# Optimization experiments

Hardware: AMD Instinct MI355X
Metric: run time of the kernel (lower is better)

## Reference

```python
import jax, jax.numpy as jnp
import numpy as np

NUM_GRAPHS = 512
LEAKY_SLOPE = 0.01


def _gconv(x, src, dst, w, W_root, W_rel, b_rel):
    # PyG GraphConv: out = lin_rel(sum_j w_ij * x_j) + lin_root(x)
    msg = x[src] * w[:, None]                       # [E, d] gather + scale
    agg = jax.ops.segment_sum(msg, dst, num_segments=x.shape[0])  # scatter-add
    return agg @ W_rel + b_rel + x @ W_root


def setup_inputs() -> dict:
    key = jax.random.key(0)
    ks = jax.random.split(key, 12)
    N, E, D, H, C = 100000, 1250000, 64, 64, 8
    x_embeddings = jax.random.normal(ks[0], (N, D), dtype=jnp.float32)
    edge_index = jax.random.randint(ks[1], (2, E), 0, N, dtype=jnp.int64)
    weights = jax.random.uniform(ks[2], (E,), dtype=jnp.float32)
    batch = jnp.sort(jax.random.randint(ks[3], (N,), 0, NUM_GRAPHS, dtype=jnp.int64))
    s1 = 1.0 / np.sqrt(D)
    s2 = 1.0 / np.sqrt(H)
    W1_root = jax.random.uniform(ks[4], (D, H), jnp.float32, -s1, s1)
    W1_rel = jax.random.uniform(ks[5], (D, H), jnp.float32, -s1, s1)
    b1 = jax.random.uniform(ks[6], (H,), jnp.float32, -s1, s1)
    W2_root = jax.random.uniform(ks[7], (H, H), jnp.float32, -s2, s2)
    W2_rel = jax.random.uniform(ks[8], (H, H), jnp.float32, -s2, s2)
    b2 = jax.random.uniform(ks[9], (H,), jnp.float32, -s2, s2)
    Wl_root = jax.random.uniform(ks[10], (H, C), jnp.float32, -s2, s2)
    bl = jax.random.uniform(ks[11], (C,), jnp.float32, -s2, s2)
    return {"x_embeddings": x_embeddings, "edge_index": edge_index,
            "weights": weights, "batch": batch,
            "W1_root": W1_root, "W1_rel": W1_rel, "b1": b1,
            "W2_root": W2_root, "W2_rel": W2_rel, "b2": b2,
            "Wl_root": Wl_root, "bl": bl}


def reference(x_embeddings, edge_index, weights, batch,
              W1_root, W1_rel, b1, W2_root, W2_rel, b2, Wl_root, bl):
    src, dst = edge_index[0], edge_index[1]
    x = _gconv(x_embeddings, src, dst, weights, W1_root, W1_rel, b1)
    x = jax.nn.leaky_relu(x, LEAKY_SLOPE)
    x = _gconv(x, src, dst, weights, W2_root, W2_rel, b2)
    x = jax.nn.leaky_relu(x, LEAKY_SLOPE)
    # global_mean_pool over graph ids
    summed = jax.ops.segment_sum(x, batch, num_segments=NUM_GRAPHS)
    counts = jax.ops.segment_sum(jnp.ones((x.shape[0],), x.dtype), batch,
                                 num_segments=NUM_GRAPHS)
    pooled = summed / jnp.maximum(counts, 1.0)[:, None]
    # final GraphConv applied with no edges: agg = 0 -> W_root x + b_rel
    out = pooled @ Wl_root + bl
    return out
```

## Files before the change

kernel.cpp:

```cpp
#include <hip/hip_runtime.h>

#define LEAKY_SLOPE 0.01f
#define NUM_GRAPHS 512
#define TILE 4096
#define NB_MAX 512
#define POOL_SPAN 8

typedef __attribute__((ext_vector_type(8))) short short8;
typedef __attribute__((ext_vector_type(4))) float f32x4;

static __device__ __forceinline__ unsigned short f2bf(float f) {
    unsigned u = __float_as_uint(f);
    u += 0x7FFFu + ((u >> 16) & 1u);
    return (unsigned short)(u >> 16);
}
static __device__ __forceinline__ float bf2f(unsigned short h) {
    return __uint_as_float(((unsigned)h) << 16);
}

static __device__ __forceinline__ int wave_incl_scan(int v, int lane) {
#pragma unroll
    for (int off = 1; off < 64; off <<= 1) {
        int t = __shfl_up(v, off, 64);
        if (lane >= off) v += t;
    }
    return v;
}

__global__ __launch_bounds__(256)
void mega_prep(const int* __restrict__ dst, int* __restrict__ bucketCnt, int E,
               int NB, int histBlocks,
               const float* __restrict__ x, unsigned short* __restrict__ xB,
               int xElems , int xBlocks,
               const float* __restrict__ W1rel, const float* __restrict__ W1root,
               const float* __restrict__ W2rel, const float* __restrict__ W2root,
               unsigned short* __restrict__ Bt1, unsigned short* __restrict__ Bt2) {
    const int bid = blockIdx.x;
    if (bid < histBlocks) {
        __shared__ int h[NB_MAX];
        for (int t = threadIdx.x; t < NB_MAX; t += 256) h[t] = 0;
        __syncthreads();
        const int base = bid * TILE;
#pragma unroll
        for (int i = 0; i < TILE / 256; ++i) {
            int e = base + i * 256 + threadIdx.x;
            if (e < E) atomicAdd(&h[dst[e] >> 8], 1);
        }
        __syncthreads();
        for (int t = threadIdx.x; t < NB; t += 256)
            if (h[t]) atomicAdd(&bucketCnt[t], h[t]);
    } else if (bid < histBlocks + xBlocks) {
        int i = (bid - histBlocks) * 256 + threadIdx.x;
        if (i < xElems) {
            float4 f = ((const float4*)x)[i];
            ushort4 o = make_ushort4(f2bf(f.x), f2bf(f.y), f2bf(f.z), f2bf(f.w));
            ((ushort4*)xB)[i] = o;
        }
    } else {
        int b2 = bid - histBlocks - xBlocks;
        for (int idx = b2 * 2048 + threadIdx.x; idx < (b2 + 1) * 2048; idx += 256) {
            int which = idx >> 13;
            int j = idx & 8191;
            int n = j >> 7, k = j & 127;
            const float* Wr = which ? W2rel : W1rel;
            const float* Wo = which ? W2root : W1root;
            float v = (k < 64) ? Wr[k * 64 + n] : Wo[(k - 64) * 64 + n];
            (which ? Bt2 : Bt1)[j] = f2bf(v);
        }
    }
}

__global__ __launch_bounds__(512)
void bscan_kernel(const int* __restrict__ bucketCnt, int* __restrict__ bucketBase,
                  int* __restrict__ cursor, int* __restrict__ rowStart,
                  float* __restrict__ pooled, int N, int E, int NB) {
    __shared__ int ws[8];
    const int t = threadIdx.x, lane = t & 63, wid = t >> 6;
    int v = (t < NB) ? bucketCnt[t] : 0;
    int s = wave_incl_scan(v, lane);
    if (lane == 63) ws[wid] = s;
    __syncthreads();
    int add = 0;
    for (int i = 0; i < wid; ++i) add += ws[i];
    if (t < NB) {
        int excl = s + add - v;
        bucketBase[t] = excl;
        cursor[t] = excl;
    }
    if (t == 0) rowStart[N] = E;
    float4 z = make_float4(0.f, 0.f, 0.f, 0.f);
#pragma unroll
    for (int i = 0; i < 16; ++i)
        ((float4*)pooled)[t * 16 + i] = z;
}

__global__ __launch_bounds__(256)
void p1b_partition(const int* __restrict__ src, const int* __restrict__ dst,
                   const float* __restrict__ w, int* __restrict__ cursor,
                   int2* __restrict__ tmp, int E, int NB) {
    __shared__ int h[NB_MAX];
    __shared__ int cur[NB_MAX];
    __shared__ int lstart[NB_MAX];
    __shared__ int gbase[NB_MAX];
    __shared__ int ws[4];
    __shared__ int2 pay[TILE];
    __shared__ unsigned short bk[TILE];

    for (int t = threadIdx.x; t < NB_MAX; t += 256) h[t] = 0;
    __syncthreads();

    const int base = blockIdx.x * TILE;
    int   myb[TILE / 256];
    int   myp[TILE / 256];
    float myw[TILE / 256];
#pragma unroll
    for (int i = 0; i < TILE / 256; ++i) {
        int e = base + i * 256 + threadIdx.x;
        if (e < E) {
            int d = dst[e];
            myb[i] = d >> 8;
            myp[i] = src[e] | ((d & 255) << 20);
            myw[i] = w[e];
            atomicAdd(&h[myb[i]], 1);
        } else {
            myb[i] = -1;
        }
    }
    __syncthreads();

    {
        const int t = threadIdx.x, lane = t & 63, wid = t >> 6;
        int a = h[2 * t], b = h[2 * t + 1];
        int s = wave_incl_scan(a + b, lane);
        if (lane == 63) ws[wid] = s;
        __syncthreads();
        int add = 0;
        for (int i = 0; i < wid; ++i) add += ws[i];
        int excl = s + add - (a + b);
        lstart[2 * t] = excl;
        lstart[2 * t + 1] = excl + a;
        cur[2 * t] = excl;
        cur[2 * t + 1] = excl + a;
    }
    __syncthreads();

#pragma unroll
    for (int i = 0; i < TILE / 256; ++i) {
        if (myb[i] >= 0) {
            int p = atomicAdd(&cur[myb[i]], 1);
            pay[p] = make_int2(myp[i], __float_as_int(myw[i]));
            bk[p] = (unsigned short)myb[i];
        }
    }
    __syncthreads();

    for (int t = threadIdx.x; t < NB; t += 256) {
        int c = h[t];
        if (c) gbase[t] = atomicAdd(&cursor[t], c);
    }
    __syncthreads();

    const int total = min(TILE, E - base);
    for (int s2 = threadIdx.x; s2 < total; s2 += 256) {
        int b2 = bk[s2];
        tmp[gbase[b2] + s2 - lstart[b2]] = pay[s2];
    }
}

__global__ __launch_bounds__(256)
void p2_build(const int2* __restrict__ tmp, const int* __restrict__ bucketBase,
              int* __restrict__ rowStart, int2* __restrict__ edata,
              int N, int E, int NB) {
    const int b = blockIdx.x;
    const int s = bucketBase[b];
    const int e2 = (b + 1 < NB) ? bucketBase[b + 1] : E;
    __shared__ int h[256];
    __shared__ int cur[256];
    __shared__ int ws[4];
    h[threadIdx.x] = 0;
    __syncthreads();
    for (int j = s + threadIdx.x; j < e2; j += 256) {
        int dl = (tmp[j].x >> 20) & 255;
        atomicAdd(&h[dl], 1);
    }
    __syncthreads();
    const int t = threadIdx.x, lane = t & 63, wid = t >> 6;
    int v = h[t];
    int sc = wave_incl_scan(v, lane);
    if (lane == 63) ws[wid] = sc;
    __syncthreads();
    int add = 0;
    for (int i = 0; i < wid; ++i) add += ws[i];
    int excl = sc + add - v;
    const int node = b * 256 + t;
    if (node < N) rowStart[node] = s + excl;
    cur[t] = excl;
    __syncthreads();
    for (int j = s + threadIdx.x; j < e2; j += 256) {
        int2 v2 = tmp[j];
        int dl = (v2.x >> 20) & 255;
        int p = atomicAdd(&cur[dl], 1);
        edata[s + p] = make_int2(v2.x & 0x1FFFF, v2.y);
    }
}

__global__ __launch_bounds__(256)
void gather_kernel(const unsigned short* __restrict__ xB, const int* __restrict__ rowStart,
                   const int2* __restrict__ edata, unsigned short* __restrict__ aggB, int N) {
    const int node = blockIdx.x * 4 + (threadIdx.x >> 6);
    if (node >= N) return;
    const int lane = threadIdx.x & 63;
    const int grp  = lane >> 4;
    const int f4   = (lane & 15) * 4;
    const int s = rowStart[node];
    const int e = rowStart[node + 1];

    float a0 = 0.f, a1 = 0.f, a2 = 0.f, a3 = 0.f;
    for (int j = s; j < e; j += 16) {
        int   idx[4];
        int2  ed[4];
#pragma unroll
        for (int u = 0; u < 4; ++u) {
            int ii = j + u * 4 + grp;
            idx[u] = (ii < e) ? ii : s;
            ed[u] = edata[idx[u]];
        }
        ushort4 r[4];
#pragma unroll
        for (int u = 0; u < 4; ++u)
            r[u] = *(const ushort4*)(xB + (size_t)ed[u].x * 64 + f4);
#pragma unroll
        for (int u = 0; u < 4; ++u) {
            int ii = j + u * 4 + grp;
            float wv = (ii < e) ? __int_as_float(ed[u].y) : 0.0f;
            a0 += bf2f(r[u].x) * wv;  a1 += bf2f(r[u].y) * wv;
            a2 += bf2f(r[u].z) * wv;  a3 += bf2f(r[u].w) * wv;
        }
    }
    a0 += __shfl_xor(a0, 16, 64);  a1 += __shfl_xor(a1, 16, 64);
    a2 += __shfl_xor(a2, 16, 64);  a3 += __shfl_xor(a3, 16, 64);
    a0 += __shfl_xor(a0, 32, 64);  a1 += __shfl_xor(a1, 32, 64);
    a2 += __shfl_xor(a2, 32, 64);  a3 += __shfl_xor(a3, 32, 64);
    if (grp == 0) {
        ushort4 o = make_ushort4(f2bf(a0), f2bf(a1), f2bf(a2), f2bf(a3));
        *(ushort4*)(aggB + (size_t)node * 64 + f4) = o;
    }
}

__global__ __launch_bounds__(256)
void transform_store(const unsigned short* __restrict__ aggB,
                     const unsigned short* __restrict__ rootB,
                     const unsigned short* __restrict__ Bt,
                     const float* __restrict__ bias,
                     unsigned short* __restrict__ xoutB, int N) {
    const int wave = threadIdx.x >> 6;
    const int lane = threadIdx.x & 63;
    const int quad = lane >> 4;
    const int l16  = lane & 15;
    const int m0   = blockIdx.x * 128 + wave * 32;

    short8 bf[4][4];
#pragma unroll
    for (int t = 0; t < 4; ++t)
#pragma unroll
        for (int k = 0; k < 4; ++k)
            bf[t][k] = *(const short8*)(Bt + (t * 16 + l16) * 128 + k * 32 + quad * 8);

    f32x4 acc[2][4];
#pragma unroll
    for (int s = 0; s < 2; ++s)
#pragma unroll
        for (int t = 0; t < 4; ++t)
            acc[s][t] = (f32x4){0.f, 0.f, 0.f, 0.f};

#pragma unroll
    for (int s = 0; s < 2; ++s) {
        int row = m0 + s * 16 + l16;
        int rowc = row < N ? row : N - 1;
        const unsigned short* arow = aggB  + (size_t)rowc * 64;
        const unsigned short* xrow = rootB + (size_t)rowc * 64;
        short8 af[4];
        af[0] = *(const short8*)(arow + quad * 8);
        af[1] = *(const short8*)(arow + 32 + quad * 8);
        af[2] = *(const short8*)(xrow + quad * 8);
        af[3] = *(const short8*)(xrow + 32 + quad * 8);
#pragma unroll
        for (int t = 0; t < 4; ++t)
#pragma unroll
            for (int k = 0; k < 4; ++k)
                acc[s][t] = __builtin_amdgcn_mfma_f32_16x16x32_bf16(bf[t][k], af[k],
                                                                    acc[s][t], 0, 0, 0);
    }

#pragma unroll
    for (int s = 0; s < 2; ++s) {
        const int node = m0 + s * 16 + l16;
        if (node < N) {
#pragma unroll
            for (int t = 0; t < 4; ++t) {
                const float4 bb = *(const float4*)(bias + t * 16 + quad * 4);
                float v0 = acc[s][t][0] + bb.x;
                float v1 = acc[s][t][1] + bb.y;
                float v2 = acc[s][t][2] + bb.z;
                float v3 = acc[s][t][3] + bb.w;
                v0 = (v0 > 0.f) ? v0 : LEAKY_SLOPE * v0;
                v1 = (v1 > 0.f) ? v1 : LEAKY_SLOPE * v1;
                v2 = (v2 > 0.f) ? v2 : LEAKY_SLOPE * v2;
                v3 = (v3 > 0.f) ? v3 : LEAKY_SLOPE * v3;
                ushort4 o = make_ushort4(f2bf(v0), f2bf(v1), f2bf(v2), f2bf(v3));
                *(ushort4*)(xoutB + (size_t)node * 64 + t * 16 + quad * 4) = o;
            }
        }
    }
}

__global__ __launch_bounds__(256)
void transform_pool(const unsigned short* __restrict__ aggB,
                    const unsigned short* __restrict__ rootB,
                    const unsigned short* __restrict__ Bt,
                    const float* __restrict__ bias,
                    const int* __restrict__ batch,
                    float* __restrict__ pooled, int N) {
    const int wave = threadIdx.x >> 6;
    const int lane = threadIdx.x & 63;
    const int quad = lane >> 4;
    const int l16  = lane & 15;
    const int m0   = blockIdx.x * 128 + wave * 32;

    __shared__ float lpool[POOL_SPAN * 64];
    const int gmin = batch[blockIdx.x * 128];
    for (int i = threadIdx.x; i < POOL_SPAN * 64; i += 256) lpool[i] = 0.f;

    short8 bf[4][4];
#pragma unroll
    for (int t = 0; t < 4; ++t)
#pragma unroll
        for (int k = 0; k < 4; ++k)
            bf[t][k] = *(const short8*)(Bt + (t * 16 + l16) * 128 + k * 32 + quad * 8);

    f32x4 acc[2][4];
#pragma unroll
    for (int s = 0; s < 2; ++s)
#pragma unroll
        for (int t = 0; t < 4; ++t)
            acc[s][t] = (f32x4){0.f, 0.f, 0.f, 0.f};

#pragma unroll
    for (int s = 0; s < 2; ++s) {
        int row = m0 + s * 16 + l16;
        int rowc = row < N ? row : N - 1;
        const unsigned short* arow = aggB  + (size_t)rowc * 64;
        const unsigned short* xrow = rootB + (size_t)rowc * 64;
        short8 af[4];
        af[0] = *(const short8*)(arow + quad * 8);
        af[1] = *(const short8*)(arow + 32 + quad * 8);
        af[2] = *(const short8*)(xrow + quad * 8);
        af[3] = *(const short8*)(xrow + 32 + quad * 8);
#pragma unroll
        for (int t = 0; t < 4; ++t)
#pragma unroll
            for (int k = 0; k < 4; ++k)
                acc[s][t] = __builtin_amdgcn_mfma_f32_16x16x32_bf16(af[k], bf[t][k],
                                                                    acc[s][t], 0, 0, 0);
    }

    __syncthreads();

#pragma unroll
    for (int s = 0; s < 2; ++s) {
#pragma unroll
        for (int t = 0; t < 4; ++t) {
            const int col = t * 16 + l16;
            const float b = bias[col];
            const int rowbase = m0 + s * 16 + quad * 4;
            float v[4]; int g[4]; int nv = 0;
#pragma unroll
            for (int r = 0; r < 4; ++r) {
                int row = rowbase + r;
                if (row < N) {
                    float a = acc[s][t][r] + b;
                    a = (a > 0.0f) ? a : LEAKY_SLOPE * a;
                    v[nv] = a;
                    g[nv] = batch[row];
                    ++nv;
                }
            }
            if (nv == 4 && g[0] == g[3]) {
                int gl = g[0] - gmin;
                float sum = v[0] + v[1] + v[2] + v[3];
                if (gl < POOL_SPAN) atomicAdd(&lpool[gl * 64 + col], sum);
                else                atomicAdd(&pooled[g[0] * 64 + col], sum);
            } else {
                for (int r = 0; r < nv; ++r) {
                    int gl = g[r] - gmin;
                    if (gl < POOL_SPAN) atomicAdd(&lpool[gl * 64 + col], v[r]);
                    else                atomicAdd(&pooled[g[r] * 64 + col], v[r]);
                }
            }
        }
    }

    __syncthreads();
    for (int i = threadIdx.x; i < POOL_SPAN * 64; i += 256) {
        float v = lpool[i];
        if (v != 0.0f)
            atomicAdd(&pooled[(gmin + (i >> 6)) * 64 + (i & 63)], v);
    }
}

__global__ __launch_bounds__(64)
void final_kernel(const float* __restrict__ pooled, const int* __restrict__ batch,
                  int N, const float* __restrict__ Wl, const float* __restrict__ bl,
                  float* __restrict__ out) {
    const int g = blockIdx.x;
    const int j = threadIdx.x;
    __shared__ float sp[64];
    __shared__ int scnt;
    if (j == 0) {
        int lo = 0, hi = N;
        while (lo < hi) { int mid = (lo + hi) >> 1; if (batch[mid] < g) lo = mid + 1; else hi = mid; }
        const int start = lo;
        hi = N;
        while (lo < hi) { int mid = (lo + hi) >> 1; if (batch[mid] < g + 1) lo = mid + 1; else hi = mid; }
        scnt = lo - start;
    }
    __syncthreads();
    const float c = fmaxf((float)scnt, 1.0f);
    sp[j] = pooled[g * 64 + j] / c;
    __syncthreads();
    if (j < 8) {
        float acc = bl[j];
#pragma unroll
        for (int k = 0; k < 64; ++k) acc += sp[k] * Wl[k * 8 + j];
        out[g * 8 + j] = acc;
    }
}

extern "C" void kernel_launch(void* const* d_in, const int* in_sizes, int n_in,
                              void* d_out, int out_size, void* d_ws, size_t ws_size,
                              hipStream_t stream) {
    const float* x      = (const float*)d_in[0];
    const int*   ei     = (const int*)  d_in[1];
    const float* w      = (const float*)d_in[2];
    const int*   batch  = (const int*)  d_in[3];
    const float* W1root = (const float*)d_in[4];
    const float* W1rel  = (const float*)d_in[5];
    const float* b1     = (const float*)d_in[6];
    const float* W2root = (const float*)d_in[7];
    const float* W2rel  = (const float*)d_in[8];
    const float* b2     = (const float*)d_in[9];
    const float* Wl     = (const float*)d_in[10];
    const float* bl     = (const float*)d_in[11];
    float* out = (float*)d_out;

    const int E = in_sizes[2];
    const int N = in_sizes[3];
    const int* src = ei;
    const int* dst = ei + E;
    const int NB = (N + 255) / 256;

    unsigned short* xB   = (unsigned short*)d_ws;
    unsigned short* aggB = xB   + (size_t)N * 64;
    unsigned short* x1B  = aggB + (size_t)N * 64;
    int2*  tmp      = (int2*)(x1B + (size_t)N * 64);
    int2*  edata    = tmp + E;
    unsigned short* Bt1 = (unsigned short*)(edata + E);
    unsigned short* Bt2 = Bt1 + 64 * 128;
    int*   rowStart = (int*)(Bt2 + 64 * 128);
    int*   bucketCnt  = rowStart + (N + 1);
    int*   bucketBase = bucketCnt + NB_MAX;
    int*   cursor     = bucketBase + NB_MAX;
    float* pooled   = (float*)(cursor + NB_MAX);

    const int histBlocks = (E + TILE - 1) / TILE;
    const int xElems = N * 16;
    const int xBlocks = (xElems + 255) / 256;

    hipMemsetAsync(bucketCnt, 0, NB_MAX * sizeof(int), stream);
    mega_prep<<<histBlocks + xBlocks + 8, 256, 0, stream>>>(
        dst, bucketCnt, E, NB, histBlocks,
        x, xB, xElems, xBlocks,
        W1rel, W1root, W2rel, W2root, Bt1, Bt2);
    bscan_kernel<<<1, 512, 0, stream>>>(bucketCnt, bucketBase, cursor, rowStart,
                                        pooled, N, E, NB);
    p1b_partition<<<histBlocks, 256, 0, stream>>>(src, dst, w, cursor, tmp, E, NB);
    p2_build<<<NB, 256, 0, stream>>>(tmp, bucketBase, rowStart, edata, N, E, NB);

    const int tBlocks = (N + 127) / 128;
    gather_kernel<<<(N + 3) / 4, 256, 0, stream>>>(xB, rowStart, edata, aggB, N);
    transform_store<<<tBlocks, 256, 0, stream>>>(aggB, xB, Bt1, b1, x1B, N);
    gather_kernel<<<(N + 3) / 4, 256, 0, stream>>>(x1B, rowStart, edata, aggB, N);
    transform_pool<<<tBlocks, 256, 0, stream>>>(aggB, x1B, Bt2, b2, batch, pooled, N);
    final_kernel<<<NUM_GRAPHS, 64, 0, stream>>>(pooled, batch, N, Wl, bl, out);
}
```

Before: 272.5 us.

## Fuse neighbor gather with MFMA transform through shared-memory aggregation tile

Merges the per-node gather kernel and the MFMA transform kernel into one templated kernel per layer. Each 512-thread block aggregates 128 nodes (16 per wave, processed serially) into a padded LDS tile, then runs the bf16 MFMA transform and the store or pooling epilogue from LDS. This removes the global aggB write and read-back plus two kernel launches. In exchange each wave walks its 16 nodes one after another before a block-wide barrier, so there are fewer independent waves to hide gather latency, and load imbalance across waves can stall the block.

After: 309.2 us. 13.5% more time.

```diff
diff --git a/kernel.cpp b/kernel.cpp
--- a/kernel.cpp
+++ b/kernel.cpp
@@ -5,6 +5,7 @@
 #define TILE 4096
 #define NB_MAX 512
 #define POOL_SPAN 8
+#define LROW 72
 
 typedef __attribute__((ext_vector_type(8))) short short8;
 typedef __attribute__((ext_vector_type(4))) float f32x4;
@@ -204,60 +205,66 @@
     }
 }
 
-__global__ __launch_bounds__(256)
-void gather_kernel(const unsigned short* __restrict__ xB, const int* __restrict__ rowStart,
-                   const int2* __restrict__ edata, unsigned short* __restrict__ aggB, int N) {
-    const int node = blockIdx.x * 4 + (threadIdx.x >> 6);
-    if (node >= N) return;
+template <bool POOL>
+__global__ __launch_bounds__(512)
+void fused_layer(const unsigned short* __restrict__ rootB,
+                 const int* __restrict__ rowStart,
+                 const int2* __restrict__ edata,
+                 const unsigned short* __restrict__ Bt,
+                 const float* __restrict__ bias,
+                 unsigned short* __restrict__ xoutB,
+                 const int* __restrict__ batch,
+                 float* __restrict__ pooled, int N) {
+    __shared__ unsigned short lagg[128 * LROW];
+    __shared__ float lpool[POOL_SPAN * 64];
+
+    const int wave = threadIdx.x >> 6;
     const int lane = threadIdx.x & 63;
     const int grp  = lane >> 4;
     const int f4   = (lane & 15) * 4;
-    const int s = rowStart[node];
-    const int e = rowStart[node + 1];
-
-    float a0 = 0.f, a1 = 0.f, a2 = 0.f, a3 = 0.f;
-    for (int j = s; j < e; j += 16) {
-        int   idx[4];
-        int2  ed[4];
-#pragma unroll
-        for (int u = 0; u < 4; ++u) {
-            int ii = j + u * 4 + grp;
-            idx[u] = (ii < e) ? ii : s;
-            ed[u] = edata[idx[u]];
-        }
-        ushort4 r[4];
-#pragma unroll
-        for (int u = 0; u < 4; ++u)
-            r[u] = *(const ushort4*)(xB + (size_t)ed[u].x * 64 + f4);
-#pragma unroll
-        for (int u = 0; u < 4; ++u) {
-            int ii = j + u * 4 + grp;
-            float wv = (ii < e) ? __int_as_float(ed[u].y) : 0.0f;
-            a0 += bf2f(r[u].x) * wv;  a1 += bf2f(r[u].y) * wv;
-            a2 += bf2f(r[u].z) * wv;  a3 += bf2f(r[u].w) * wv;
-        }
-    }
-    a0 += __shfl_xor(a0, 16, 64);  a1 += __shfl_xor(a1, 16, 64);
-    a2 += __shfl_xor(a2, 16, 64);  a3 += __shfl_xor(a3, 16, 64);
-    a0 += __shfl_xor(a0, 32, 64);  a1 += __shfl_xor(a1, 32, 64);
-    a2 += __shfl_xor(a2, 32, 64);  a3 += __shfl_xor(a3, 32, 64);
-    if (grp == 0) {
-        ushort4 o = make_ushort4(f2bf(a0), f2bf(a1), f2bf(a2), f2bf(a3));
-        *(ushort4*)(aggB + (size_t)node * 64 + f4) = o;
-    }
-}
-
-__global__ __launch_bounds__(256)
-void transform_store(const unsigned short* __restrict__ aggB,
-                     const unsigned short* __restrict__ rootB,
-                     const unsigned short* __restrict__ Bt,
-                     const float* __restrict__ bias,
-                     unsigned short* __restrict__ xoutB, int N) {
-    const int wave = threadIdx.x >> 6;
-    const int lane = threadIdx.x & 63;
     const int quad = lane >> 4;
     const int l16  = lane & 15;
-    const int m0   = blockIdx.x * 128 + wave * 32;
+    const int m0   = blockIdx.x * 128;
+
+    if (POOL) {
+        for (int i = threadIdx.x; i < POOL_SPAN * 64; i += 512) lpool[i] = 0.f;
+    }
+
+    for (int n = 0; n < 16; ++n) {
+        const int node = m0 + wave * 16 + n;
+        if (node >= N) break;
+        const int s = rowStart[node];
+        const int e = rowStart[node + 1];
+        float a0 = 0.f, a1 = 0.f, a2 = 0.f, a3 = 0.f;
+        for (int j = s; j < e; j += 16) {
+            int2 ed[4];
+#pragma unroll
+            for (int u = 0; u < 4; ++u) {
+                int ii = j + u * 4 + grp;
+                ed[u] = edata[(ii < e) ? ii : s];
+            }
+            ushort4 r[4];
+#pragma unroll
+            for (int u = 0; u < 4; ++u)
+                r[u] = *(const ushort4*)(rootB + (size_t)ed[u].x * 64 + f4);
+#pragma unroll
+            for (int u = 0; u < 4; ++u) {
+                int ii = j + u * 4 + grp;
+                float wv = (ii < e) ? __int_as_float(ed[u].y) : 0.0f;
+                a0 += bf2f(r[u].x) * wv;  a1 += bf2f(r[u].y) * wv;
+                a2 += bf2f(r[u].z) * wv;  a3 += bf2f(r[u].w) * wv;
+            }
+        }
+        a0 += __shfl_xor(a0, 16, 64);  a1 += __shfl_xor(a1, 16, 64);
+        a2 += __shfl_xor(a2, 16, 64);  a3 += __shfl_xor(a3, 16, 64);
+        a0 += __shfl_xor(a0, 32, 64);  a1 += __shfl_xor(a1, 32, 64);
+        a2 += __shfl_xor(a2, 32, 64);  a3 += __shfl_xor(a3, 32, 64);
+        if (grp == 0) {
+            ushort4 o = make_ushort4(f2bf(a0), f2bf(a1), f2bf(a2), f2bf(a3));
+            *(ushort4*)(lagg + (wave * 16 + n) * LROW + f4) = o;
+        }
+    }
+    __syncthreads();
 
     short8 bf[4][4];
 #pragma unroll
@@ -266,43 +273,35 @@
         for (int k = 0; k < 4; ++k)
             bf[t][k] = *(const short8*)(Bt + (t * 16 + l16) * 128 + k * 32 + quad * 8);
 
-    f32x4 acc[2][4];
-#pragma unroll
-    for (int s = 0; s < 2; ++s)
+    f32x4 acc[4];
+#pragma unroll
+    for (int t = 0; t < 4; ++t) acc[t] = (f32x4){0.f, 0.f, 0.f, 0.f};
+
+    const int row = m0 + wave * 16 + l16;
+    const int rowc = row < N ? row : N - 1;
+    const unsigned short* xrow = rootB + (size_t)rowc * 64;
+    short8 af[4];
+    af[0] = *(const short8*)(lagg + (wave * 16 + l16) * LROW + quad * 8);
+    af[1] = *(const short8*)(lagg + (wave * 16 + l16) * LROW + 32 + quad * 8);
+    af[2] = *(const short8*)(xrow + quad * 8);
+    af[3] = *(const short8*)(xrow + 32 + quad * 8);
+
+    if (!POOL) {
 #pragma unroll
         for (int t = 0; t < 4; ++t)
-            acc[s][t] = (f32x4){0.f, 0.f, 0.f, 0.f};
-
-#pragma unroll
-    for (int s = 0; s < 2; ++s) {
-        int row = m0 + s * 16 + l16;
-        int rowc = row < N ? row : N - 1;
-        const unsigned short* arow = aggB  + (size_t)rowc * 64;
-        const unsigned short* xrow = rootB + (size_t)rowc * 64;
-        short8 af[4];
-        af[0] = *(const short8*)(arow + quad * 8);
-        af[1] = *(const short8*)(arow + 32 + quad * 8);
-        af[2] = *(const short8*)(xrow + quad * 8);
-        af[3] = *(const short8*)(xrow + 32 + quad * 8);
-#pragma unroll
-        for (int t = 0; t < 4; ++t)
 #pragma unroll
             for (int k = 0; k < 4; ++k)
-                acc[s][t] = __builtin_amdgcn_mfma_f32_16x16x32_bf16(bf[t][k], af[k],
-                                                                    acc[s][t], 0, 0, 0);
-    }
-
-#pragma unroll
-    for (int s = 0; s < 2; ++s) {
-        const int node = m0 + s * 16 + l16;
+                acc[t] = __builtin_amdgcn_mfma_f32_16x16x32_bf16(bf[t][k], af[k],
+                                                                 acc[t], 0, 0, 0);
+        const int node = m0 + wave * 16 + l16;
         if (node < N) {
 #pragma unroll
             for (int t = 0; t < 4; ++t) {
                 const float4 bb = *(const float4*)(bias + t * 16 + quad * 4);
-                float v0 = acc[s][t][0] + bb.x;
-                float v1 = acc[s][t][1] + bb.y;
-                float v2 = acc[s][t][2] + bb.z;
-                float v3 = acc[s][t][3] + bb.w;
+                float v0 = acc[t][0] + bb.x;
+                float v1 = acc[t][1] + bb.y;
+                float v2 = acc[t][2] + bb.z;
+                float v3 = acc[t][3] + bb.w;
                 v0 = (v0 > 0.f) ? v0 : LEAKY_SLOPE * v0;
                 v1 = (v1 > 0.f) ? v1 : LEAKY_SLOPE * v1;
                 v2 = (v2 > 0.f) ? v2 : LEAKY_SLOPE * v2;
@@ -311,77 +310,28 @@
                 *(ushort4*)(xoutB + (size_t)node * 64 + t * 16 + quad * 4) = o;
             }
         }
-    }
-}
-
-__global__ __launch_bounds__(256)
-void transform_pool(const unsigned short* __restrict__ aggB,
-                    const unsigned short* __restrict__ rootB,
-                    const unsigned short* __restrict__ Bt,
-                    const float* __restrict__ bias,
-                    const int* __restrict__ batch,
-                    float* __restrict__ pooled, int N) {
-    const int wave = threadIdx.x >> 6;
-    const int lane = threadIdx.x & 63;
-    const int quad = lane >> 4;
-    const int l16  = lane & 15;
-    const int m0   = blockIdx.x * 128 + wave * 32;
-
-    __shared__ float lpool[POOL_SPAN * 64];
-    const int gmin = batch[blockIdx.x * 128];
-    for (int i = threadIdx.x; i < POOL_SPAN * 64; i += 256) lpool[i] = 0.f;
-
-    short8 bf[4][4];
-#pragma unroll
-    for (int t = 0; t < 4; ++t)
-#pragma unroll
-        for (int k = 0; k < 4; ++k)
-            bf[t][k] = *(const short8*)(Bt + (t * 16 + l16) * 128 + k * 32 + quad * 8);
-
-    f32x4 acc[2][4];
-#pragma unroll
-    for (int s = 0; s < 2; ++s)
+    } else {
 #pragma unroll
         for (int t = 0; t < 4; ++t)
-            acc[s][t] = (f32x4){0.f, 0.f, 0.f, 0.f};
-
-#pragma unroll
-    for (int s = 0; s < 2; ++s) {
-        int row = m0 + s * 16 + l16;
-        int rowc = row < N ? row : N - 1;
-        const unsigned short* arow = aggB  + (size_t)rowc * 64;
-        const unsigned short* xrow = rootB + (size_t)rowc * 64;
-        short8 af[4];
-        af[0] = *(const short8*)(arow + quad * 8);
-        af[1] = *(const short8*)(arow + 32 + quad * 8);
-        af[2] = *(const short8*)(xrow + quad * 8);
-        af[3] = *(const short8*)(xrow + 32 + quad * 8);
-#pragma unroll
-        for (int t = 0; t < 4; ++t)
 #pragma unroll
             for (int k = 0; k < 4; ++k)
-                acc[s][t] = __builtin_amdgcn_mfma_f32_16x16x32_bf16(af[k], bf[t][k],
-                                                                    acc[s][t], 0, 0, 0);
-    }
-
-    __syncthreads();
-
-#pragma unroll
-    for (int s = 0; s < 2; ++s) {
+                acc[t] = __builtin_amdgcn_mfma_f32_16x16x32_bf16(af[k], bf[t][k],
+                                                                 acc[t], 0, 0, 0);
+        const int gmin = batch[m0];
 #pragma unroll
         for (int t = 0; t < 4; ++t) {
             const int col = t * 16 + l16;
             const float b = bias[col];
-            const int rowbase = m0 + s * 16 + quad * 4;
+            const int rowbase = m0 + wave * 16 + quad * 4;
             float v[4]; int g[4]; int nv = 0;
 #pragma unroll
             for (int r = 0; r < 4; ++r) {
-                int row = rowbase + r;
-                if (row < N) {
-                    float a = acc[s][t][r] + b;
+                int rr = rowbase + r;
+                if (rr < N) {
+                    float a = acc[t][r] + b;
                     a = (a > 0.0f) ? a : LEAKY_SLOPE * a;
                     v[nv] = a;
-                    g[nv] = batch[row];
+                    g[nv] = batch[rr];
                     ++nv;
                 }
             }
@@ -398,13 +348,12 @@
                 }
             }
         }
-    }
-
-    __syncthreads();
-    for (int i = threadIdx.x; i < POOL_SPAN * 64; i += 256) {
-        float v = lpool[i];
-        if (v != 0.0f)
-            atomicAdd(&pooled[(gmin + (i >> 6)) * 64 + (i & 63)], v);
+        __syncthreads();
+        for (int i = threadIdx.x; i < POOL_SPAN * 64; i += 512) {
+            float vv = lpool[i];
+            if (vv != 0.0f)
+                atomicAdd(&pooled[(gmin + (i >> 6)) * 64 + (i & 63)], vv);
+        }
     }
 }
 
@@ -460,8 +409,7 @@
     const int NB = (N + 255) / 256;
 
     unsigned short* xB   = (unsigned short*)d_ws;
-    unsigned short* aggB = xB   + (size_t)N * 64;
-    unsigned short* x1B  = aggB + (size_t)N * 64;
+    unsigned short* x1B  = xB + (size_t)N * 64;
     int2*  tmp      = (int2*)(x1B + (size_t)N * 64);
     int2*  edata    = tmp + E;
     unsigned short* Bt1 = (unsigned short*)(edata + E);
@@ -487,9 +435,9 @@
     p2_build<<<NB, 256, 0, stream>>>(tmp, bucketBase, rowStart, edata, N, E, NB);
 
     const int tBlocks = (N + 127) / 128;
-    gather_kernel<<<(N + 3) / 4, 256, 0, stream>>>(xB, rowStart, edata, aggB, N);
-    transform_store<<<tBlocks, 256, 0, stream>>>(aggB, xB, Bt1, b1, x1B, N);
-    gather_kernel<<<(N + 3) / 4, 256, 0, stream>>>(x1B, rowStart, edata, aggB, N);
-    transform_pool<<<tBlocks, 256, 0, stream>>>(aggB, x1B, Bt2, b2, batch, pooled, N);
+    fused_layer<false><<<tBlocks, 512, 0, stream>>>(xB, rowStart, edata, Bt1, b1,
+                                                    x1B, nullptr, nullptr, N);
+    fused_layer<true><<<tBlocks, 512, 0, stream>>>(x1B, rowStart, edata, Bt2, b2,
+                                                   nullptr, batch, pooled, N);
     final_kernel<<<NUM_GRAPHS, 64, 0, stream>>>(pooled, batch, N, Wl, bl, out);
 }
```
